# Optimization experiments

Hardware: AMD Instinct MI355X
Metric: run time of the kernel (lower is better)

Reference implementation:

```python
import jax, jax.numpy as jnp
import numpy as np
from jax.scipy.stats import norm as jnorm

B, S, D, H, E, K, FF = 8, 256, 1024, 16, 4, 2, 4096
HD = D // H
NOISE_EPS = 0.01
LOSS_COEF = 0.01
EPS_FILL = float(np.finfo(float).eps)


def _ln(x, g, b):
    m = x.mean(-1, keepdims=True)
    v = x.var(-1, keepdims=True)
    return (x - m) * jax.lax.rsqrt(v + 1e-5) * g + b


def setup_inputs() -> dict:
    key = jax.random.key(0)
    ks = jax.random.split(key, 16)
    r = lambda i, shape, s=1.0: jax.random.normal(ks[i], shape, dtype=jnp.float32) * s
    return {
        "x": r(0, (B, S, D)),
        "e_outputs": r(1, (B, 64, D)),            # unused (is_lm=True) but part of signature
        "noise": r(2, (B, E)),                     # the randn_like(clean_logits) draw
        "w_gate": r(3, (D, E), 0.02),
        "w_noise": r(4, (D, E), 0.02),
        "Wq": r(5, (E, D, D), 0.02),
        "Wk": r(6, (E, D, D), 0.02),
        "Wv": r(7, (E, D, D), 0.02),
        "Wo": r(8, (E, D, D), 0.02),
        "W1": r(9, (E, D, FF), 0.02),
        "b1": jnp.zeros((E, FF), jnp.float32),
        "W2": r(10, (E, FF, D), 0.02),
        "b2": jnp.zeros((E, D), jnp.float32),
        "g1": jnp.ones((E, D), jnp.float32),
        "be1": jnp.zeros((E, D), jnp.float32),
        "g2": jnp.ones((E, D), jnp.float32),
        "be2": jnp.zeros((E, D), jnp.float32),
        "trg_mask": jnp.tril(jnp.ones((S, S), dtype=bool))[None, None],  # causal [1,1,S,S]
        "src_mask": jnp.ones((1, 1, 1, 64), dtype=bool),                 # unused (is_lm=True)
    }


def _cv_squared(v):
    # torch .var() is unbiased (ddof=1)
    return v.var(ddof=1) / (v.mean() ** 2 + 1e-10)


def reference(x, e_outputs, noise, w_gate, w_noise, Wq, Wk, Wv, Wo, W1, b1, W2, b2,
              g1, be1, g2, be2, trg_mask, src_mask):
    b, s, d = x.shape
    # ---- noisy top-k gating (per sample, on the sequence-sum) ----
    xs = x.sum(axis=1)                                   # [B, D]
    clean = xs @ w_gate                                  # [B, E]
    raw_noise = xs @ w_noise                             # [B, E]
    stddev = jax.nn.softplus(raw_noise) + NOISE_EPS      # train=True -> *1.0
    noisy = clean + noise * stddev                       # logits
    top_logits, top_idx = jax.lax.top_k(noisy, K + 1)    # [B, K+1]
    topk_gates = jax.nn.softmax(top_logits[:, :K], axis=1)
    gates = jnp.zeros_like(noisy).at[jnp.arange(b)[:, None], top_idx[:, :K]].set(topk_gates)
    # load: prob each expert's clean logit lands in the noisy top-k
    thr_in = top_logits[:, K:K + 1]                      # (k+1)-th noisy value
    thr_out = top_logits[:, K - 1:K]                     # k-th noisy value
    is_in = noisy > thr_in
    prob = jnp.where(is_in,
                     jnorm.cdf((clean - thr_in) / stddev),
                     jnorm.cdf((clean - thr_out) / stddev))
    load = prob.sum(0)                                   # [E]
    importance = gates.sum(0)                            # [E]
    loss = (_cv_squared(importance) + _cv_squared(load)) * LOSS_COEF

    # ---- experts: standard decoder layer (self-attn + FFN), is_lm -> no cross-attn ----
    neg = jnp.asarray(-1e9, x.dtype)
    scale = 1.0 / np.sqrt(HD)

    def expert(p):
        wq, wk, wv, wo, w1, bb1, w2, bb2, gg1, bbe1, gg2, bbe2 = p
        q = (x @ wq).reshape(b, s, H, HD)
        k_ = (x @ wk).reshape(b, s, H, HD)
        v = (x @ wv).reshape(b, s, H, HD)
        scores = jnp.einsum('bqhd,bkhd->bhqk', q, k_) * scale
        scores = jnp.where(trg_mask, scores, neg)
        attn = jax.nn.softmax(scores, axis=-1)
        o = jnp.einsum('bhqk,bkhd->bqhd', attn, v).reshape(b, s, d) @ wo
        h = _ln(x + o, gg1, bbe1)
        ff = jax.nn.relu(h @ w1 + bb1) @ w2 + bb2
        return _ln(h + ff, gg2, bbe2)

    outs = jax.vmap(expert)((Wq, Wk, Wv, Wo, W1, b1, W2, b2, g1, be1, g2, be2))  # [E,B,S,D]

    # ---- combine: scatter-add of gate-weighted expert outputs (dense equivalent) ----
    y = jnp.einsum('be,ebsd->bsd', gates, outs)
    y = jnp.where(y == 0, jnp.asarray(EPS_FILL, y.dtype), y)
    return y, loss
```

## Files before the change

kernel.cpp:

```cpp
#include <hip/hip_runtime.h>
#include <hip/hip_bf16.h>

typedef __bf16 bf16;
typedef __attribute__((ext_vector_type(4))) __bf16 bf16x4;
typedef __attribute__((ext_vector_type(8))) __bf16 bf16x8;
typedef __attribute__((ext_vector_type(4))) float floatx4;

constexpr int CB = 8, CS = 256, CD = 1024, CH = 16, CE = 4, CFF = 4096, CHD = 64;
constexpr long long DD  = 1048576;
constexpr long long DFF = 4194304;
constexpr long long BSD = 2097152;
constexpr long long PSD = 4194304;

constexpr size_t OFF_PART = 0;
constexpr size_t OFF_CLEAN= 262144;
constexpr size_t OFF_RAW  = 262272;
constexpr size_t OFF_GATES= 262400;
constexpr size_t OFF_EACT = 262528;
constexpr size_t OFF_PBE  = 262592;
constexpr size_t OFF_BP   = 262656;
constexpr size_t OFF_XBF  = 263168;
constexpr size_t OFF_WT   = OFF_XBF + (size_t)BSD*2;
constexpr size_t OFF_W1T  = OFF_WT  + (size_t)16*DD*2;
constexpr size_t OFF_W2T  = OFF_W1T + (size_t)4*DFF*2;
constexpr size_t OFF_QKV  = OFF_W2T + (size_t)4*DFF*2;
constexpr size_t OFF_AO   = OFF_QKV + (size_t)3*PSD*2;
constexpr size_t OFF_F1   = OFF_QKV;
constexpr size_t OFF_PB   = OFF_AO  + (size_t)PSD*2;
constexpr size_t OFF_VT   = OFF_PB;
constexpr size_t OFF_H    = OFF_PB  + (size_t)2*PSD*4;
constexpr size_t OFF_HBF  = OFF_H   + (size_t)PSD*4;

__global__ __launch_bounds__(256)
void wtrans_cvt(const float* __restrict__ Wq, const float* __restrict__ Wk,
                const float* __restrict__ Wv, const float* __restrict__ Wo,
                const float* __restrict__ W1, const float* __restrict__ W2,
                bf16* __restrict__ wT, bf16* __restrict__ w1T, bf16* __restrict__ w2T,
                const float* __restrict__ x, bf16* __restrict__ xbf, float* __restrict__ part) {
  int zb = blockIdx.x;
  if (zb >= 3072) {
    int blk = zb - 3072;
    int b = blk >> 3, ch = blk & 7;
    int t = threadIdx.x;
    float s0 = 0.f, s1 = 0.f, s2 = 0.f, s3 = 0.f;
    long long base4 = ((long long)(b*CS + ch*32))*CD / 4;
#pragma unroll 4
    for (int r = 0; r < 32; ++r) {
      long long i4 = base4 + (long long)r*(CD/4) + t;
      float4 v = ((const float4*)x)[i4];
      bf16x4 o; o[0] = (bf16)v.x; o[1] = (bf16)v.y; o[2] = (bf16)v.z; o[3] = (bf16)v.w;
      ((bf16x4*)xbf)[i4] = o;
      s0 += v.x; s1 += v.y; s2 += v.z; s3 += v.w;
    }
    float4 sv; sv.x = s0; sv.y = s1; sv.z = s2; sv.w = s3;
    ((float4*)(part + (long long)blk*CD))[t] = sv;
    return;
  }
  int w = threadIdx.x >> 6;
  const float* src; bf16* d; int rows, cols, btk, btn;
  if (zb < 1024) {
    int m = zb >> 6, bt = zb & 63; int e = m >> 2; int which = m & 3;
    src = ((which == 0) ? Wq : (which == 1) ? Wk : (which == 2) ? Wv : Wo) + (long long)e*DD;
    d = wT + (long long)m*DD; rows = 1024; cols = 1024;
    btk = bt >> 3; btn = bt & 7;
  } else if (zb < 2048) {
    int z2 = zb - 1024; int e = z2 >> 8; int bt = z2 & 255;
    src = W1 + (long long)e*DFF; d = w1T + (long long)e*DFF;
    rows = 1024; cols = 4096; btk = bt >> 5; btn = bt & 31;
  } else {
    int z3 = zb - 2048; int e = z3 >> 8; int bt = z3 & 255;
    src = W2 + (long long)e*DFF; d = w2T + (long long)e*DFF;
    rows = 4096; cols = 1024; btk = bt >> 3; btn = bt & 7;
  }
  int tk = btk*2 + (w & 1);
  int tn = btn*2 + (w >> 1);
  int lane = threadIdx.x & 63;
  int ln = lane >> 3, lk = lane & 7;
  int k0 = tk*64, n0 = tn*64;
  const float* s = src + (long long)(k0 + lk*8)*cols + n0 + ln*8;
  floatx4 f[8][2];
#pragma unroll
  for (int j = 0; j < 8; ++j) {
    f[j][0] = __builtin_nontemporal_load((const floatx4*)(s + (long long)j*cols));
    f[j][1] = __builtin_nontemporal_load((const floatx4*)(s + (long long)j*cols + 4));
  }
  bf16* dp = d + (long long)(n0 + ln*8)*rows + k0 + lk*8;
#pragma unroll
  for (int jn = 0; jn < 8; ++jn) {
    bf16x8 o;
#pragma unroll
    for (int jk = 0; jk < 8; ++jk) {
      o[jk] = (bf16)f[jk][jn >> 2][jn & 3];
    }
    *(bf16x8*)(dp + (long long)jn*rows) = o;
  }
}

__global__ __launch_bounds__(256)
void gate_dots(const float* __restrict__ part, const float* __restrict__ wg,
               const float* __restrict__ wn, float* __restrict__ clean, float* __restrict__ raw) {
  int p = blockIdx.x, b = p >> 2, e = p & 3;
  int t = threadIdx.x;
  float s1 = 0.f, s2 = 0.f;
  for (int d = t; d < CD; d += 256) {
    float xv = 0.f;
#pragma unroll
    for (int c = 0; c < 8; ++c) xv += part[(long long)(b*8 + c)*CD + d];
    s1 += xv * wg[d*CE + e];
    s2 += xv * wn[d*CE + e];
  }
  for (int off = 32; off; off >>= 1) { s1 += __shfl_xor(s1, off); s2 += __shfl_xor(s2, off); }
  __shared__ float r1[4], r2[4];
  int lane = t & 63, w = t >> 6;
  if (lane == 0) { r1[w] = s1; r2[w] = s2; }
  __syncthreads();
  if (t == 0) { clean[p] = r1[0]+r1[1]+r1[2]+r1[3]; raw[p] = r2[0]+r2[1]+r2[2]+r2[3]; }
}

__global__ void gating_kernel(const float* __restrict__ clean, const float* __restrict__ raw,
                              const float* __restrict__ noise, float* __restrict__ gates,
                              int* __restrict__ eact, int* __restrict__ pairBE,
                              int* __restrict__ batchPair, float* __restrict__ loss_out) {
  if (threadIdx.x != 0) return;
  float imp[CE] = {0,0,0,0}, load[CE] = {0,0,0,0};
  int act[CE] = {0,0,0,0};
  for (int b = 0; b < CB; ++b) {
    float cl[CE], sd[CE], ny[CE];
    for (int e = 0; e < CE; ++e) {
      cl[e] = clean[b*CE + e];
      float rw = raw[b*CE + e];
      float sp = fmaxf(rw, 0.f) + log1pf(expf(-fabsf(rw)));
      sd[e] = sp + 0.01f;
      ny[e] = cl[e] + noise[b*CE + e]*sd[e];
    }
    int idx[CE] = {0,1,2,3};
    for (int a = 0; a < 3; ++a) {
      int best = a;
      for (int c = a + 1; c < 4; ++c) if (ny[idx[c]] > ny[idx[best]]) best = c;
      int tt = idx[a]; idx[a] = idx[best]; idx[best] = tt;
    }
    float l0 = ny[idx[0]], l1 = ny[idx[1]], l2 = ny[idx[2]];
    float e1 = expf(l1 - l0);
    float g0 = 1.f/(1.f + e1), g1v = e1/(1.f + e1);
    for (int e = 0; e < CE; ++e) gates[b*CE + e] = 0.f;
    gates[b*CE + idx[0]] = g0; gates[b*CE + idx[1]] = g1v;
    imp[idx[0]] += g0; imp[idx[1]] += g1v;
    act[idx[0]] = 1; act[idx[1]] = 1;
    for (int e = 0; e < CE; ++e) {
      bool is_in = ny[e] > l2;
      float thr = is_in ? l2 : l1;
      float zz = (cl[e] - thr) / sd[e];
      load[e] += 0.5f * erfcf(-zz * 0.70710678118654752440f);
    }
  }
  int pe2p[CB][CE];
  int pc = 0;
  for (int e = 0; e < CE; ++e)
    for (int b = 0; b < CB; ++b)
      if (gates[b*CE + e] != 0.f) { pairBE[pc] = b | (e << 8); pe2p[b][e] = pc; ++pc; }
  for (int b = 0; b < CB; ++b) {
    int s = 0;
    for (int e = 0; e < CE; ++e)
      if (gates[b*CE + e] != 0.f) batchPair[2*b + (s++)] = pe2p[b][e];
  }
  float m1 = 0.f, m2 = 0.f;
  for (int e = 0; e < CE; ++e) { m1 += imp[e]; m2 += load[e]; }
  m1 *= 0.25f; m2 *= 0.25f;
  float v1 = 0.f, v2 = 0.f;
  for (int e = 0; e < CE; ++e) { float d1 = imp[e]-m1, d2 = load[e]-m2; v1 += d1*d1; v2 += d2*d2; }
  v1 *= (1.f/3.f); v2 *= (1.f/3.f);
  loss_out[0] = 0.01f * (v1/(m1*m1 + 1e-10f) + v2/(m2*m2 + 1e-10f));
  for (int e = 0; e < CE; ++e) eact[e] = act[e];
}

__global__ __launch_bounds__(256)
void transpose_v(const bf16* __restrict__ qkvC, bf16* __restrict__ vTb) {
  int z = blockIdx.x; int p = z >> 4, h = z & 15;
  int w = threadIdx.x >> 6, lane = threadIdx.x & 63;
  int ln = lane >> 3, lk = lane & 7;
  const bf16* v = qkvC + 2*PSD + ((long long)(p*CS + w*64 + ln*8))*CD + h*CHD + lk*8;
  bf16x8 in[8];
#pragma unroll
  for (int j = 0; j < 8; ++j) in[j] = *(const bf16x8*)(v + (long long)j*CD);
  bf16* vt = vTb + ((long long)(p*CH + h)*CHD + lk*8)*CS + w*64 + ln*8;
#pragma unroll
  for (int dn = 0; dn < 8; ++dn) {
    bf16x8 o;
#pragma unroll
    for (int j = 0; j < 8; ++j) o[j] = in[j][dn];
    *(bf16x8*)(vt + (long long)dn*CS) = o;
  }
}

__device__ __forceinline__ void cp16(const bf16* g, bf16* l) {
  __builtin_amdgcn_global_load_lds((const __attribute__((address_space(1))) void*)g,
                                   (__attribute__((address_space(3))) void*)l, 16, 0, 0);
}

template<int R, int W, int NT>
__device__ __forceinline__ void stageN(const bf16* __restrict__ src, int ld, bf16* dst) {
  constexpr int W8 = W/8;
  int t = threadIdx.x;
  int l = t & 63, wid = t >> 6;
#pragma unroll
  for (int i = 0; i < (R*W8)/NT; ++i) {
    int idb = i*NT + wid*64;
    int id = idb + l;
    int row = id / W8, sl = id % W8;
    int gc = sl ^ (row & 7);
    cp16(src + (long long)row*ld + gc*8, dst + (long long)idb*8);
  }
}

__global__ __launch_bounds__(256)
void attn_fused(const bf16* __restrict__ qkvC, const bf16* __restrict__ vTb,
                bf16* __restrict__ aoC) {
  int h = blockIdx.x, p = blockIdx.y, qt = blockIdx.z;
  const bf16* qp = qkvC + (long long)(p*CS)*CD + h*CHD;
  const bf16* kp = qp + PSD;
  const bf16* vt = vTb + (long long)(p*CH + h)*CHD*CS;
  bf16* aop = aoC + (long long)(p*CS)*CD + h*CHD;

  __shared__ bf16 Ps[64*264];
  __shared__ float smaxL[64*4], ssumL[64*4], Lrow[64];

  int t = threadIdx.x, w = t >> 6, lane = t & 63, lr = lane & 15, quad = lane >> 4;

  floatx4 accs[4][4] = {};
  if (w <= qt) {
#pragma unroll
    for (int kk = 0; kk < 2; ++kk) {
      int c = kk*4 + quad;
      bf16x8 af[4], bfr[4];
#pragma unroll
      for (int i = 0; i < 4; ++i) {
        af[i]  = *(const bf16x8*)(qp + (long long)(qt*64 + i*16 + lr)*CD + c*8);
        bfr[i] = *(const bf16x8*)(kp + (long long)(w*64  + i*16 + lr)*CD + c*8);
      }
#pragma unroll
      for (int i = 0; i < 4; ++i)
#pragma unroll
        for (int j = 0; j < 4; ++j)
          accs[i][j] = __builtin_amdgcn_mfma_f32_16x16x32_bf16(af[i], bfr[j], accs[i][j], 0, 0, 0);
    }
  }
  float rmax[4][4];
#pragma unroll
  for (int i = 0; i < 4; ++i)
#pragma unroll
    for (int r = 0; r < 4; ++r) {
      int qrow = qt*64 + i*16 + quad*4 + r;
      float m = -3.0e38f;
#pragma unroll
      for (int j = 0; j < 4; ++j) {
        int kcol = w*64 + j*16 + lr;
        float s = accs[i][j][r]*0.125f;
        s = (kcol <= qrow) ? s : -3.0e38f;
        accs[i][j][r] = s;
        m = fmaxf(m, s);
      }
      rmax[i][r] = m;
    }
#pragma unroll
  for (int off = 1; off <= 8; off <<= 1)
#pragma unroll
    for (int i = 0; i < 4; ++i)
#pragma unroll
      for (int r = 0; r < 4; ++r) rmax[i][r] = fmaxf(rmax[i][r], __shfl_xor(rmax[i][r], off));
  if (lr == 0)
#pragma unroll
    for (int i = 0; i < 4; ++i)
#pragma unroll
      for (int r = 0; r < 4; ++r) smaxL[(i*16 + quad*4 + r)*4 + w] = rmax[i][r];
  __syncthreads();
  float rsum[4][4];
#pragma unroll
  for (int i = 0; i < 4; ++i)
#pragma unroll
    for (int r = 0; r < 4; ++r) {
      floatx4 mv = *(const floatx4*)&smaxL[(i*16 + quad*4 + r)*4];
      float M = fmaxf(fmaxf(mv[0], mv[1]), fmaxf(mv[2], mv[3]));
      float srow = 0.f;
#pragma unroll
      for (int j = 0; j < 4; ++j) {
        float pp = __expf(accs[i][j][r] - M);
        accs[i][j][r] = pp;
        srow += pp;
      }
      rsum[i][r] = srow;
    }
#pragma unroll
  for (int off = 1; off <= 8; off <<= 1)
#pragma unroll
    for (int i = 0; i < 4; ++i)
#pragma unroll
      for (int r = 0; r < 4; ++r) rsum[i][r] += __shfl_xor(rsum[i][r], off);
  if (lr == 0)
#pragma unroll
    for (int i = 0; i < 4; ++i)
#pragma unroll
      for (int r = 0; r < 4; ++r) ssumL[(i*16 + quad*4 + r)*4 + w] = rsum[i][r];
  __syncthreads();
  if (w == 0 && lr == 0) {
#pragma unroll
    for (int i = 0; i < 4; ++i)
#pragma unroll
      for (int r = 0; r < 4; ++r) {
        int m = i*16 + quad*4 + r;
        floatx4 sv = *(const floatx4*)&ssumL[m*4];
        Lrow[m] = sv[0] + sv[1] + sv[2] + sv[3];
      }
  }
  if (w <= qt) {
#pragma unroll
    for (int i = 0; i < 4; ++i)
#pragma unroll
      for (int j = 0; j < 4; ++j)
#pragma unroll
        for (int r = 0; r < 4; ++r)
          Ps[(i*16 + quad*4 + r)*264 + w*64 + j*16 + lr] = (bf16)accs[i][j][r];
  }
  __syncthreads();
  floatx4 acco[4] = {};
  int ksMax = (qt + 1)*2;
  for (int ks = 0; ks < ksMax; ++ks) {
    int c = ks*4 + quad;
    bf16x8 ap = *(const bf16x8*)(Ps + (w*16 + lr)*264 + c*8);
#pragma unroll
    for (int j = 0; j < 4; ++j) {
      bf16x8 bv = *(const bf16x8*)(vt + (long long)(j*16 + lr)*CS + c*8);
      acco[j] = __builtin_amdgcn_mfma_f32_16x16x32_bf16(ap, bv, acco[j], 0, 0, 0);
    }
  }
#pragma unroll
  for (int r = 0; r < 4; ++r) {
    int orow = w*16 + quad*4 + r;
    float inv = 1.f / Lrow[orow];
#pragma unroll
    for (int j = 0; j < 4; ++j)
      aop[(long long)(qt*64 + orow)*CD + j*16 + lr] = (bf16)(acco[j][r]*inv);
  }
}

__global__ __launch_bounds__(256)
void ln1_kernel(const float* __restrict__ x, const float* __restrict__ PbF,
                const float* __restrict__ gamma, const float* __restrict__ beta,
                float* __restrict__ h, bf16* __restrict__ hbf, const int* __restrict__ pairBE) {
  int row = blockIdx.x;
  int pbe = pairBE[row >> 8]; int pb = pbe & 255, pe = pbe >> 8;
  int t = threadIdx.x;
  float4 a = ((const float4*)(x + ((long long)pb*CS + (row & 255))*CD))[t];
  float4 b = ((const float4*)(PbF + (long long)row*CD))[t];
  float4 c = ((const float4*)(PbF + PSD + (long long)row*CD))[t];
  float v0 = a.x + b.x + c.x, v1 = a.y + b.y + c.y;
  float v2 = a.z + b.z + c.z, v3 = a.w + b.w + c.w;
  float s  = v0 + v1 + v2 + v3;
  float s2 = v0*v0 + v1*v1 + v2*v2 + v3*v3;
  int lane = t & 63, wave = t >> 6;
  for (int off = 32; off; off >>= 1) { s += __shfl_xor(s, off); s2 += __shfl_xor(s2, off); }
  __shared__ float red[8];
  if (lane == 0) { red[wave*2] = s; red[wave*2 + 1] = s2; }
  __syncthreads();
  s  = red[0] + red[2] + red[4] + red[6];
  s2 = red[1] + red[3] + red[5] + red[7];
  float mean = s * (1.f/CD);
  float rstd = rsqrtf(s2*(1.f/CD) - mean*mean + 1e-5f);
  float4 gm = ((const float4*)(gamma + (long long)pe*CD))[t];
  float4 bt = ((const float4*)(beta  + (long long)pe*CD))[t];
  float4 o;
  o.x = (v0 - mean)*rstd*gm.x + bt.x;
  o.y = (v1 - mean)*rstd*gm.y + bt.y;
  o.z = (v2 - mean)*rstd*gm.z + bt.z;
  o.w = (v3 - mean)*rstd*gm.w + bt.w;
  ((float4*)(h + (long long)row*CD))[t] = o;
  bf16x4 ob; ob[0] = (bf16)o.x; ob[1] = (bf16)o.y; ob[2] = (bf16)o.z; ob[3] = (bf16)o.w;
  ((bf16x4*)(hbf + (long long)row*CD))[t] = ob;
}

__global__ __launch_bounds__(256)
void ln2y_kernel(const float* __restrict__ h, const bf16* __restrict__ PbB,
                 const float* __restrict__ gamma, const float* __restrict__ beta,
                 float* __restrict__ y, const float* __restrict__ gates,
                 const int* __restrict__ pairBE, const int* __restrict__ batchPair) {
  int row = blockIdx.x;
  int b = row >> 8, sIdx = row & 255;
  int p0 = batchPair[2*b], p1 = batchPair[2*b + 1];
  int e0 = pairBE[p0] >> 8, e1 = pairBE[p1] >> 8;
  float gv0 = gates[b*CE + e0], gv1 = gates[b*CE + e1];
  long long r0 = (long long)p0*CS + sIdx, r1 = (long long)p1*CS + sIdx;
  int t = threadIdx.x;
  float4 a = ((const float4*)(h + r0*CD))[t];
  float4 c = ((const float4*)(h + r1*CD))[t];
#pragma unroll
  for (int k = 0; k < 4; ++k) {
    bf16x4 pa = ((const bf16x4*)(PbB + (long long)k*PSD + r0*CD))[t];
    bf16x4 pc = ((const bf16x4*)(PbB + (long long)k*PSD + r1*CD))[t];
    a.x += (float)pa[0]; a.y += (float)pa[1]; a.z += (float)pa[2]; a.w += (float)pa[3];
    c.x += (float)pc[0]; c.y += (float)pc[1]; c.z += (float)pc[2]; c.w += (float)pc[3];
  }
  float sA = a.x + a.y + a.z + a.w;
  float sA2 = a.x*a.x + a.y*a.y + a.z*a.z + a.w*a.w;
  float sB = c.x + c.y + c.z + c.w;
  float sB2 = c.x*c.x + c.y*c.y + c.z*c.z + c.w*c.w;
  int lane = t & 63, wave = t >> 6;
  for (int off = 32; off; off >>= 1) {
    sA += __shfl_xor(sA, off); sA2 += __shfl_xor(sA2, off);
    sB += __shfl_xor(sB, off); sB2 += __shfl_xor(sB2, off);
  }
  __shared__ float red[16];
  if (lane == 0) { red[wave*4] = sA; red[wave*4+1] = sA2; red[wave*4+2] = sB; red[wave*4+3] = sB2; }
  __syncthreads();
  sA  = red[0] + red[4] + red[8]  + red[12];
  sA2 = red[1] + red[5] + red[9]  + red[13];
  sB  = red[2] + red[6] + red[10] + red[14];
  sB2 = red[3] + red[7] + red[11] + red[15];
  float mA = sA*(1.f/CD), mB = sB*(1.f/CD);
  float rsA = rsqrtf(sA2*(1.f/CD) - mA*mA + 1e-5f);
  float rsB = rsqrtf(sB2*(1.f/CD) - mB*mB + 1e-5f);
  float4 gm0 = ((const float4*)(gamma + (long long)e0*CD))[t];
  float4 bt0 = ((const float4*)(beta  + (long long)e0*CD))[t];
  float4 gm1 = ((const float4*)(gamma + (long long)e1*CD))[t];
  float4 bt1 = ((const float4*)(beta  + (long long)e1*CD))[t];
  float4 o;
  o.x = gv0*((a.x - mA)*rsA*gm0.x + bt0.x) + gv1*((c.x - mB)*rsB*gm1.x + bt1.x);
  o.y = gv0*((a.y - mA)*rsA*gm0.y + bt0.y) + gv1*((c.y - mB)*rsB*gm1.y + bt1.y);
  o.z = gv0*((a.z - mA)*rsA*gm0.z + bt0.z) + gv1*((c.z - mB)*rsB*gm1.z + bt1.z);
  o.w = gv0*((a.w - mA)*rsA*gm0.w + bt0.w) + gv1*((c.w - mB)*rsB*gm1.w + bt1.w);
  constexpr float EF = 2.2204460492503131e-16f;
  o.x = (o.x == 0.f) ? EF : o.x;  o.y = (o.y == 0.f) ? EF : o.y;
  o.z = (o.z == 0.f) ? EF : o.z;  o.w = (o.w == 0.f) ? EF : o.w;
  ((float4*)(y + (long long)row*CD))[t] = o;
}

enum { EPI_BF16 = 0, EPI_F32 = 1, EPI_BRELU = 2, EPI_BIASBF16 = 3 };

template<int EPI, int KS, bool A_BATCH>
__global__ __launch_bounds__(512, 2)
void gemm_nt(const bf16* __restrict__ A, const bf16* __restrict__ Bt, void* __restrict__ Cv,
             int K , int lda, int ldb, int ldc,
             long long oBe, long long oBmat, long long oCmat, long long oCk,
             const float* __restrict__ bias, long long biasStride,
             const int* __restrict__ pairBE) {
  constexpr int BM = 256, BN = 256;
  int z = blockIdx.z;
  int zk = z % KS, mat = z / KS;
  int gx = gridDim.x;
  int nwg = gx * gridDim.y;
  int lin = blockIdx.x + gx*blockIdx.y;
  int nl  = (lin & 7)*(nwg >> 3) + (lin >> 3);
  int m0 = (nl % gx) * BM, n0 = (nl / gx) * BN;
  int pbe = pairBE[m0 >> 8]; int pb = pbe & 255, pe = pbe >> 8;
  const bf16* Ab = A + (A_BATCH ? ((long long)pb*CS + (m0 & 255))*lda : (long long)m0*lda)
                     + (long long)zk*K;
  const bf16* Bb = Bt + (long long)pe*oBe + (long long)mat*oBmat + (long long)zk*K
                      + (long long)n0*ldb;
  long long coff = (long long)mat*oCmat + (long long)zk*oCk;

  __shared__ bf16 As[2][BM*64];
  __shared__ bf16 Bs[2][BN*64];

  int wave = threadIdx.x >> 6;
  int lane = threadIdx.x & 63;
  int wm = wave >> 2, wn = wave & 3;
  int lr = lane & 15;
  int quad = lane >> 4;

  floatx4 acc[8][4] = {};

  int nt = K / 64;
  stageN<BM, 64, 512>(Ab, lda, As[0]);
  stageN<BN, 64, 512>(Bb, ldb, Bs[0]);
  for (int t = 0; t < nt; ++t) {
    int cur = t & 1;
    if (t + 1 < nt) {
      stageN<BM, 64, 512>(Ab + (t+1)*64, lda, As[cur ^ 1]);
      stageN<BN, 64, 512>(Bb + (t+1)*64, ldb, Bs[cur ^ 1]);
      asm volatile("s_waitcnt vmcnt(8)" ::: "memory");
    } else {
      asm volatile("s_waitcnt vmcnt(0)" ::: "memory");
    }
    __builtin_amdgcn_s_barrier();
    asm volatile("" ::: "memory");
#pragma unroll
    for (int kk = 0; kk < 2; ++kk) {
      int c = kk*4 + quad;
      bf16x8 af[8], bfr[4];
#pragma unroll
      for (int i = 0; i < 8; ++i) {
        int m = wm*128 + i*16 + lr;
        af[i] = *(const bf16x8*)(As[cur] + m*64 + ((c ^ (m & 7))*8));
      }
#pragma unroll
      for (int j = 0; j < 4; ++j) {
        int n = wn*64 + j*16 + lr;
        bfr[j] = *(const bf16x8*)(Bs[cur] + n*64 + ((c ^ (n & 7))*8));
      }
#pragma unroll
      for (int i = 0; i < 8; ++i)
#pragma unroll
        for (int j = 0; j < 4; ++j)
          acc[i][j] = __builtin_amdgcn_mfma_f32_16x16x32_bf16(af[i], bfr[j], acc[i][j], 0, 0, 0);
    }
    __builtin_amdgcn_s_barrier();
    asm volatile("" ::: "memory");
  }

#pragma unroll
  for (int j = 0; j < 4; ++j) {
    int col = n0 + wn*64 + j*16 + lr;
    float bv = 0.f;
    if constexpr (EPI == EPI_BRELU || EPI == EPI_BIASBF16)
      if (zk == 0) bv = bias[(long long)pe*biasStride + col];
#pragma unroll
    for (int i = 0; i < 8; ++i) {
#pragma unroll
      for (int r = 0; r < 4; ++r) {
        int row = m0 + wm*128 + i*16 + quad*4 + r;
        float v = acc[i][j][r] + bv;
        long long idx = coff + (long long)row*ldc + col;
        if constexpr (EPI == EPI_BF16)          ((bf16*)Cv)[idx] = (bf16)v;
        else if constexpr (EPI == EPI_F32)      ((float*)Cv)[idx] = v;
        else if constexpr (EPI == EPI_BRELU)    ((bf16*)Cv)[idx] = (bf16)fmaxf(v, 0.f);
        else                                    ((bf16*)Cv)[idx] = (bf16)v;
      }
    }
  }
}

extern "C" void kernel_launch(void* const* d_in, const int* in_sizes, int n_in,
                              void* d_out, int out_size, void* d_ws, size_t ws_size,
                              hipStream_t stream) {
  const float* x       = (const float*)d_in[0];
  const float* noise   = (const float*)d_in[2];
  const float* w_gate  = (const float*)d_in[3];
  const float* w_noise = (const float*)d_in[4];
  const float* Wq      = (const float*)d_in[5];
  const float* Wk      = (const float*)d_in[6];
  const float* Wv      = (const float*)d_in[7];
  const float* Wo      = (const float*)d_in[8];
  const float* W1      = (const float*)d_in[9];
  const float* b1      = (const float*)d_in[10];
  const float* W2      = (const float*)d_in[11];
  const float* b2      = (const float*)d_in[12];
  const float* g1      = (const float*)d_in[13];
  const float* be1     = (const float*)d_in[14];
  const float* g2      = (const float*)d_in[15];
  const float* be2     = (const float*)d_in[16];

  char* ws = (char*)d_ws;
  float* y    = (float*)d_out;
  float* loss = y + (size_t)BSD;

  float* part  = (float*)(ws + OFF_PART);
  float* clean = (float*)(ws + OFF_CLEAN);
  float* raw   = (float*)(ws + OFF_RAW);
  float* gates = (float*)(ws + OFF_GATES);
  int*   eact  = (int*)  (ws + OFF_EACT);
  int*   pairBE= (int*)  (ws + OFF_PBE);
  int*   batchPair = (int*)(ws + OFF_BP);
  bf16*  xbf   = (bf16*) (ws + OFF_XBF);
  bf16*  wT    = (bf16*) (ws + OFF_WT);
  bf16*  w1T   = (bf16*) (ws + OFF_W1T);
  bf16*  w2T   = (bf16*) (ws + OFF_W2T);
  bf16*  qkvC  = (bf16*) (ws + OFF_QKV);
  bf16*  aoC   = (bf16*) (ws + OFF_AO);
  bf16*  f1    = (bf16*) (ws + OFF_F1);
  bf16*  vTb   = (bf16*) (ws + OFF_VT);
  float* PbF   = (float*)(ws + OFF_PB);
  bf16*  PbB   = (bf16*) (ws + OFF_PB);
  float* h     = (float*)(ws + OFF_H);
  bf16*  hbf   = (bf16*) (ws + OFF_HBF);

  wtrans_cvt<<<3136, 256, 0, stream>>>(Wq, Wk, Wv, Wo, W1, W2, wT, w1T, w2T, x, xbf, part);
  gate_dots<<<32, 256, 0, stream>>>(part, w_gate, w_noise, clean, raw);
  gating_kernel<<<1, 64, 0, stream>>>(clean, raw, noise, gates, eact, pairBE, batchPair, loss);

  gemm_nt<EPI_BF16, 1, true><<<dim3(16, 4, 3), 512, 0, stream>>>(
      xbf, wT, qkvC, 1024, 1024, 1024, 1024,
      4*DD, DD, PSD, 0, nullptr, 0, pairBE);

  transpose_v<<<256, 256, 0, stream>>>(qkvC, vTb);

  attn_fused<<<dim3(CH, 16, 4), 256, 0, stream>>>(qkvC, vTb, aoC);

  gemm_nt<EPI_F32, 2, false><<<dim3(16, 4, 2), 512, 0, stream>>>(
      aoC, wT + 3*DD, PbF, 512, 1024, 1024, 1024,
      4*DD, 0, 0, PSD, nullptr, 0, pairBE);

  ln1_kernel<<<4096, 256, 0, stream>>>(x, PbF, g1, be1, h, hbf, pairBE);

  gemm_nt<EPI_BRELU, 1, false><<<dim3(16, 16, 1), 512, 0, stream>>>(
      hbf, w1T, f1, 1024, 1024, 1024, 4096,
      DFF, 0, 0, 0, b1, CFF, pairBE);

  gemm_nt<EPI_BIASBF16, 4, false><<<dim3(16, 4, 4), 512, 0, stream>>>(
      f1, w2T, PbB, 1024, 4096, 4096, 1024,
      DFF, 0, 0, PSD, b2, CD, pairBE);

  ln2y_kernel<<<2048, 256, 0, stream>>>(h, PbB, g2, be2, y, gates, pairBE, batchPair);
}
```

Before: 488.9 us.

## Add 128-row triple-buffered GEMM tiles for QKV/Wo and fuse gating kernels

The GEMM kernel is templated on the M tile size. A 128-row variant uses a three-stage shared-memory pipeline with adjusted vmcnt waits, and the QKV and output-projection GEMMs switch to it. This doubles their workgroup count so more of the CUs are busy on these small GEMMs, at the cost of more reloading of B tiles and a larger LDS footprint. Separately, the gate dot products and the top-k gating logic are merged into one single-block kernel, removing a launch and a round-trip through global memory.

```diff
diff --git a/kernel.cpp b/kernel.cpp
--- a/kernel.cpp
+++ b/kernel.cpp
@@ -97,31 +97,51 @@
 }
 
 __global__ __launch_bounds__(256)
-void gate_dots(const float* __restrict__ part, const float* __restrict__ wg,
-               const float* __restrict__ wn, float* __restrict__ clean, float* __restrict__ raw) {
-  int p = blockIdx.x, b = p >> 2, e = p & 3;
+void gate_fused(const float* __restrict__ part, const float* __restrict__ wg,
+                const float* __restrict__ wn, const float* __restrict__ noise,
+                float* __restrict__ gates, int* __restrict__ eact, int* __restrict__ pairBE,
+                int* __restrict__ batchPair, float* __restrict__ loss_out) {
   int t = threadIdx.x;
-  float s1 = 0.f, s2 = 0.f;
-  for (int d = t; d < CD; d += 256) {
-    float xv = 0.f;
-#pragma unroll
-    for (int c = 0; c < 8; ++c) xv += part[(long long)(b*8 + c)*CD + d];
-    s1 += xv * wg[d*CE + e];
-    s2 += xv * wn[d*CE + e];
-  }
-  for (int off = 32; off; off >>= 1) { s1 += __shfl_xor(s1, off); s2 += __shfl_xor(s2, off); }
-  __shared__ float r1[4], r2[4];
-  int lane = t & 63, w = t >> 6;
-  if (lane == 0) { r1[w] = s1; r2[w] = s2; }
+  float4 wgv[4], wnv[4];
+  float xv[CB][4];
+#pragma unroll
+  for (int k = 0; k < 4; ++k) {
+    int d = t + k*256;
+    wgv[k] = ((const float4*)wg)[d];
+    wnv[k] = ((const float4*)wn)[d];
+#pragma unroll
+    for (int b = 0; b < CB; ++b) {
+      float s = 0.f;
+#pragma unroll
+      for (int c = 0; c < 8; ++c) s += part[(long long)(b*8 + c)*CD + d];
+      xv[b][k] = s;
+    }
+  }
+  __shared__ float red[4][64];
+  __shared__ float sCR[64];
+  int lane = t & 63, wv = t >> 6;
+#pragma unroll
+  for (int b = 0; b < CB; ++b) {
+#pragma unroll
+    for (int e = 0; e < CE; ++e) {
+      float s1 = 0.f, s2 = 0.f;
+#pragma unroll
+      for (int k = 0; k < 4; ++k) {
+        const float* g  = (const float*)&wgv[k];
+        const float* nn = (const float*)&wnv[k];
+        s1 += xv[b][k]*g[e];
+        s2 += xv[b][k]*nn[e];
+      }
+      for (int off = 32; off; off >>= 1) { s1 += __shfl_xor(s1, off); s2 += __shfl_xor(s2, off); }
+      if (lane == 0) { red[wv][b*4 + e] = s1; red[wv][32 + b*4 + e] = s2; }
+    }
+  }
   __syncthreads();
-  if (t == 0) { clean[p] = r1[0]+r1[1]+r1[2]+r1[3]; raw[p] = r2[0]+r2[1]+r2[2]+r2[3]; }
-}
-
-__global__ void gating_kernel(const float* __restrict__ clean, const float* __restrict__ raw,
-                              const float* __restrict__ noise, float* __restrict__ gates,
-                              int* __restrict__ eact, int* __restrict__ pairBE,
-                              int* __restrict__ batchPair, float* __restrict__ loss_out) {
-  if (threadIdx.x != 0) return;
+  if (t < 64) sCR[t] = red[0][t] + red[1][t] + red[2][t] + red[3][t];
+  __syncthreads();
+  if (t != 0) return;
+  const float* clean = sCR;
+  const float* raw   = sCR + 32;
   float imp[CE] = {0,0,0,0}, load[CE] = {0,0,0,0};
   int act[CE] = {0,0,0,0};
   for (int b = 0; b < CB; ++b) {
@@ -434,14 +454,17 @@
 
 enum { EPI_BF16 = 0, EPI_F32 = 1, EPI_BRELU = 2, EPI_BIASBF16 = 3 };
 
-template<int EPI, int KS, bool A_BATCH>
+template<int EPI, int KS, bool A_BATCH, int BM>
 __global__ __launch_bounds__(512, 2)
 void gemm_nt(const bf16* __restrict__ A, const bf16* __restrict__ Bt, void* __restrict__ Cv,
              int K , int lda, int ldb, int ldc,
              long long oBe, long long oBmat, long long oCmat, long long oCk,
              const float* __restrict__ bias, long long biasStride,
              const int* __restrict__ pairBE) {
-  constexpr int BM = 256, BN = 256;
+  constexpr int BN = 256;
+  constexpr int NBUF = (BM == 128) ? 3 : 2;
+  constexpr int DEPTH = NBUF - 1;
+  constexpr int MI = BM / 32;
   int z = blockIdx.z;
   int zk = z % KS, mat = z / KS;
   int gx = gridDim.x;
@@ -456,8 +479,8 @@
                       + (long long)n0*ldb;
   long long coff = (long long)mat*oCmat + (long long)zk*oCk;
 
-  __shared__ bf16 As[2][BM*64];
-  __shared__ bf16 Bs[2][BN*64];
+  __shared__ bf16 As[NBUF][BM*64];
+  __shared__ bf16 Bs[NBUF][BN*64];
 
   int wave = threadIdx.x >> 6;
   int lane = threadIdx.x & 63;
@@ -465,17 +488,25 @@
   int lr = lane & 15;
   int quad = lane >> 4;
 
-  floatx4 acc[8][4] = {};
+  floatx4 acc[MI][4] = {};
 
   int nt = K / 64;
-  stageN<BM, 64, 512>(Ab, lda, As[0]);
-  stageN<BN, 64, 512>(Bb, ldb, Bs[0]);
+#pragma unroll
+  for (int d = 0; d < DEPTH; ++d) {
+    stageN<BM, 64, 512>(Ab + d*64, lda, As[d]);
+    stageN<BN, 64, 512>(Bb + d*64, ldb, Bs[d]);
+  }
+  int cur = 0, stg = DEPTH;
   for (int t = 0; t < nt; ++t) {
-    int cur = t & 1;
-    if (t + 1 < nt) {
-      stageN<BM, 64, 512>(Ab + (t+1)*64, lda, As[cur ^ 1]);
-      stageN<BN, 64, 512>(Bb + (t+1)*64, ldb, Bs[cur ^ 1]);
-      asm volatile("s_waitcnt vmcnt(8)" ::: "memory");
+    if (t + DEPTH < nt) {
+      stageN<BM, 64, 512>(Ab + (t+DEPTH)*64, lda, As[stg]);
+      stageN<BN, 64, 512>(Bb + (t+DEPTH)*64, ldb, Bs[stg]);
+      if (++stg == NBUF) stg = 0;
+      if constexpr (BM == 128) asm volatile("s_waitcnt vmcnt(12)" ::: "memory");
+      else                     asm volatile("s_waitcnt vmcnt(8)"  ::: "memory");
+    } else if (t + 1 < nt) {
+      if constexpr (BM == 128) asm volatile("s_waitcnt vmcnt(6)"  ::: "memory");
+      else                     asm volatile("s_waitcnt vmcnt(0)"  ::: "memory");
     } else {
       asm volatile("s_waitcnt vmcnt(0)" ::: "memory");
     }
@@ -484,10 +515,10 @@
 #pragma unroll
     for (int kk = 0; kk < 2; ++kk) {
       int c = kk*4 + quad;
-      bf16x8 af[8], bfr[4];
-#pragma unroll
-      for (int i = 0; i < 8; ++i) {
-        int m = wm*128 + i*16 + lr;
+      bf16x8 af[MI], bfr[4];
+#pragma unroll
+      for (int i = 0; i < MI; ++i) {
+        int m = wm*(BM/2) + i*16 + lr;
         af[i] = *(const bf16x8*)(As[cur] + m*64 + ((c ^ (m & 7))*8));
       }
 #pragma unroll
@@ -496,11 +527,12 @@
         bfr[j] = *(const bf16x8*)(Bs[cur] + n*64 + ((c ^ (n & 7))*8));
       }
 #pragma unroll
-      for (int i = 0; i < 8; ++i)
+      for (int i = 0; i < MI; ++i)
 #pragma unroll
         for (int j = 0; j < 4; ++j)
           acc[i][j] = __builtin_amdgcn_mfma_f32_16x16x32_bf16(af[i], bfr[j], acc[i][j], 0, 0, 0);
     }
+    if (++cur == NBUF) cur = 0;
     __builtin_amdgcn_s_barrier();
     asm volatile("" ::: "memory");
   }
@@ -512,10 +544,10 @@
     if constexpr (EPI == EPI_BRELU || EPI == EPI_BIASBF16)
       if (zk == 0) bv = bias[(long long)pe*biasStride + col];
 #pragma unroll
-    for (int i = 0; i < 8; ++i) {
+    for (int i = 0; i < MI; ++i) {
 #pragma unroll
       for (int r = 0; r < 4; ++r) {
-        int row = m0 + wm*128 + i*16 + quad*4 + r;
+        int row = m0 + wm*(BM/2) + i*16 + quad*4 + r;
         float v = acc[i][j][r] + bv;
         long long idx = coff + (long long)row*ldc + col;
         if constexpr (EPI == EPI_BF16)          ((bf16*)Cv)[idx] = (bf16)v;
@@ -552,8 +584,6 @@
   float* loss = y + (size_t)BSD;
 
   float* part  = (float*)(ws + OFF_PART);
-  float* clean = (float*)(ws + OFF_CLEAN);
-  float* raw   = (float*)(ws + OFF_RAW);
   float* gates = (float*)(ws + OFF_GATES);
   int*   eact  = (int*)  (ws + OFF_EACT);
   int*   pairBE= (int*)  (ws + OFF_PBE);
@@ -572,10 +602,9 @@
   bf16*  hbf   = (bf16*) (ws + OFF_HBF);
 
   wtrans_cvt<<<3136, 256, 0, stream>>>(Wq, Wk, Wv, Wo, W1, W2, wT, w1T, w2T, x, xbf, part);
-  gate_dots<<<32, 256, 0, stream>>>(part, w_gate, w_noise, clean, raw);
-  gating_kernel<<<1, 64, 0, stream>>>(clean, raw, noise, gates, eact, pairBE, batchPair, loss);
-
-  gemm_nt<EPI_BF16, 1, true><<<dim3(16, 4, 3), 512, 0, stream>>>(
+  gate_fused<<<1, 256, 0, stream>>>(part, w_gate, w_noise, noise, gates, eact, pairBE, batchPair, loss);
+
+  gemm_nt<EPI_BF16, 1, true, 128><<<dim3(32, 4, 3), 512, 0, stream>>>(
       xbf, wT, qkvC, 1024, 1024, 1024, 1024,
       4*DD, DD, PSD, 0, nullptr, 0, pairBE);
 
@@ -583,17 +612,17 @@
 
   attn_fused<<<dim3(CH, 16, 4), 256, 0, stream>>>(qkvC, vTb, aoC);
 
-  gemm_nt<EPI_F32, 2, false><<<dim3(16, 4, 2), 512, 0, stream>>>(
+  gemm_nt<EPI_F32, 2, false, 128><<<dim3(32, 4, 2), 512, 0, stream>>>(
       aoC, wT + 3*DD, PbF, 512, 1024, 1024, 1024,
       4*DD, 0, 0, PSD, nullptr, 0, pairBE);
 
   ln1_kernel<<<4096, 256, 0, stream>>>(x, PbF, g1, be1, h, hbf, pairBE);
 
-  gemm_nt<EPI_BRELU, 1, false><<<dim3(16, 16, 1), 512, 0, stream>>>(
+  gemm_nt<EPI_BRELU, 1, false, 256><<<dim3(16, 16, 1), 512, 0, stream>>>(
       hbf, w1T, f1, 1024, 1024, 1024, 4096,
       DFF, 0, 0, 0, b1, CFF, pairBE);
 
-  gemm_nt<EPI_BIASBF16, 4, false><<<dim3(16, 4, 4), 512, 0, stream>>>(
+  gemm_nt<EPI_BIASBF16, 4, false, 256><<<dim3(16, 4, 4), 512, 0, stream>>>(
       f1, w2T, PbB, 1024, 4096, 4096, 1024,
       DFF, 0, 0, PSD, b2, CD, pairBE);
 
```

Result: no change. 496.4 us (+1.5%).
